# Optimization experiments

Measured on AMD Instinct MI355X. Metric: run time of the kernel, lower is better.

The kernel has to match this reference:

```python
import jax, jax.numpy as jnp
import numpy as np

L, B, S, D, H, FF, V, P = 6, 8, 1024, 768, 12, 3072, 50257, 1024
DH = D // H
EPS = 1e-5


def setup_inputs() -> dict:
    key = jax.random.key(0)
    ks = jax.random.split(key, 12)
    std = 0.02
    return {
        "x_ids": jax.random.randint(ks[0], (B, S), 0, V),
        "calibrated_mask": jax.random.normal(ks[1], (B, S, S), jnp.float32),
        "wte": jax.random.normal(ks[2], (V, D), jnp.float32) * std,
        "wpe": jax.random.normal(ks[3], (P, D), jnp.float32) * std,
        "ln1_g": jnp.ones((L, D), jnp.float32),
        "ln1_b": jnp.zeros((L, D), jnp.float32),
        "qkv_w": jax.random.normal(ks[4], (L, D, 3 * D), jnp.float32) * std,
        "qkv_b": jnp.zeros((L, 3 * D), jnp.float32),
        "ao_w": jax.random.normal(ks[5], (L, D, D), jnp.float32) * std,
        "ao_b": jnp.zeros((L, D), jnp.float32),
        "ln2_g": jnp.ones((L, D), jnp.float32),
        "ln2_b": jnp.zeros((L, D), jnp.float32),
        "fc_w": jax.random.normal(ks[6], (L, D, FF), jnp.float32) * std,
        "fc_b": jnp.zeros((L, FF), jnp.float32),
        "op_w": jax.random.normal(ks[7], (L, FF, D), jnp.float32) * std,
        "op_b": jnp.zeros((L, D), jnp.float32),
        "lnf_g": jnp.ones((D,), jnp.float32),
        "lnf_b": jnp.zeros((D,), jnp.float32),
    }


def _ln(x, g, b):
    m = jnp.mean(x, axis=-1, keepdims=True)
    v = jnp.var(x, axis=-1, keepdims=True)
    return (x - m) * jax.lax.rsqrt(v + EPS) * g + b


def _gelu_new(x):
    c = np.sqrt(2.0 / np.pi).astype(np.float32)
    return 0.5 * x * (1.0 + jnp.tanh(c * (x + 0.044715 * x * x * x)))


def _gpt2_forward(x_ids, calibrated_mask, wte, wpe, ln1_g, ln1_b, qkv_w, qkv_b,
                  ao_w, ao_b, ln2_g, ln2_b, fc_w, fc_b, op_w, op_b, lnf_g, lnf_b):
    s = x_ids.shape[1]
    h = wte[x_ids] + wpe[:s][None, :, :]  # [B,S,D]
    causal = jnp.tril(jnp.ones((s, s), bool))
    neg = jnp.finfo(h.dtype).min
    # additive mask, broadcast over heads (unsqueeze(1).repeat over n_head)
    add_mask = calibrated_mask[:, None, :, :]  # [B,1,S,S]

    def block(hid, p):
        l1g, l1b, qw, qb, aw, ab, l2g, l2b, fw, fb, ow, ob = p
        x = _ln(hid, l1g, l1b)
        qkv = x @ qw + qb  # [B,S,3D]
        q, k, v = jnp.split(qkv, 3, axis=-1)
        q = q.reshape(q.shape[0], s, H, DH).transpose(0, 2, 1, 3)
        k = k.reshape(k.shape[0], s, H, DH).transpose(0, 2, 1, 3)
        v = v.reshape(v.shape[0], s, H, DH).transpose(0, 2, 1, 3)
        scores = jnp.einsum('bhqd,bhkd->bhqk', q, k) / jnp.sqrt(jnp.asarray(DH, q.dtype))
        scores = jnp.where(causal[None, None], scores, neg)
        scores = scores + add_mask
        w = jax.nn.softmax(scores, axis=-1)
        a = jnp.einsum('bhqk,bhkd->bhqd', w, v)
        a = a.transpose(0, 2, 1, 3).reshape(a.shape[0], s, D)
        hid = hid + a @ aw + ab
        x2 = _ln(hid, l2g, l2b)
        hid = hid + _gelu_new(x2 @ fw + fb) @ ow + ob
        return hid, None

    params = (ln1_g, ln1_b, qkv_w, qkv_b, ao_w, ao_b, ln2_g, ln2_b, fc_w, fc_b, op_w, op_b)
    h, _ = jax.lax.scan(block, h, params)
    return _ln(h, lnf_g, lnf_b)


def reference(x_ids, calibrated_mask, wte, wpe, ln1_g, ln1_b, qkv_w, qkv_b,
              ao_w, ao_b, ln2_g, ln2_b, fc_w, fc_b, op_w, op_b, lnf_g, lnf_b):
    return _gpt2_forward(x_ids, calibrated_mask, wte, wpe, ln1_g, ln1_b, qkv_w, qkv_b,
                         ao_w, ao_b, ln2_g, ln2_b, fc_w, fc_b, op_w, op_b, lnf_g, lnf_b)
```

## Files before the change

### kernel.cpp

```cpp
#include <hip/hip_runtime.h>
#include <hip/hip_bf16.h>

typedef __bf16 bf16_t;
typedef __bf16 bf16x8 __attribute__((ext_vector_type(8)));
typedef float  f32x4  __attribute__((ext_vector_type(4)));

#define DEV __device__ __forceinline__

DEV void gload_lds16(const void* g, void* l) {
  __builtin_amdgcn_global_load_lds(
      (__attribute__((address_space(1))) void*)(void*)g,
      (__attribute__((address_space(3))) void*)l, 16, 0, 0);
}

__global__ __launch_bounds__(256)
void transpose_cast(const float* __restrict__ in, bf16_t* __restrict__ out,
                    int K, int N) {
  __shared__ float tile[32][33];
  const int k0 = blockIdx.x * 32;
  const int n0 = blockIdx.y * 32;
  const int tx = threadIdx.x;
  const int ty = threadIdx.y;
#pragma unroll
  for (int i = 0; i < 32; i += 8)
    tile[ty + i][tx] = in[(long)(k0 + ty + i) * N + n0 + tx];
  __syncthreads();
#pragma unroll
  for (int i = 0; i < 32; i += 8)
    out[(long)(n0 + ty + i) * K + k0 + tx] = (bf16_t)tile[tx][ty + i];
}

__global__ __launch_bounds__(256)
void embed_kernel(const int* __restrict__ ids, const float* __restrict__ wte,
                  const float* __restrict__ wpe, float* __restrict__ h) {
  const int idx = blockIdx.x * 256 + threadIdx.x;
  const int col = idx % 768;
  const int row = idx / 768;
  const int s   = row & 1023;
  h[idx] = wte[(long)ids[row] * 768 + col] + wpe[s * 768 + col];
}

template <bool BF16OUT>
__global__ __launch_bounds__(256)
void ln_kernel(const float* __restrict__ x, const float* __restrict__ g,
               const float* __restrict__ b, bf16_t* __restrict__ ob,
               float* __restrict__ of) {
  const long row = blockIdx.x;
  const float* xr = x + row * 768;
  const int t = threadIdx.x;
  float v0 = xr[t], v1 = xr[t + 256], v2 = xr[t + 512];
  float s  = v0 + v1 + v2;
  float sq = v0 * v0 + v1 * v1 + v2 * v2;
#pragma unroll
  for (int o = 32; o; o >>= 1) { s += __shfl_down(s, o); sq += __shfl_down(sq, o); }
  __shared__ float red[8];
  const int w = t >> 6;
  if ((t & 63) == 0) { red[w] = s; red[4 + w] = sq; }
  __syncthreads();
  s  = red[0] + red[1] + red[2] + red[3];
  sq = red[4] + red[5] + red[6] + red[7];
  const float mean = s * (1.f / 768.f);
  const float rs = rsqrtf(sq * (1.f / 768.f) - mean * mean + 1e-5f);
  float vv[3] = {v0, v1, v2};
#pragma unroll
  for (int i = 0; i < 3; ++i) {
    const int col = t + i * 256;
    const float o2 = (vv[i] - mean) * rs * g[col] + b[col];
    if (BF16OUT) ob[row * 768 + col] = (bf16_t)o2;
    else         of[row * 768 + col] = o2;
  }
}

template <int EPI, int BN>
__global__ __launch_bounds__(256, 4)
void gemm_bt(const bf16_t* __restrict__ A, const bf16_t* __restrict__ Bt,
             const float* __restrict__ bias, float* __restrict__ Cf,
             bf16_t* __restrict__ Cb, int M, int N, int K) {
  constexpr int NI = BN / 32;
  __shared__ bf16_t As[128 * 64];
  __shared__ bf16_t Bs[BN * 64];
  const int tid  = threadIdx.x;
  const int lane = tid & 63, w = tid >> 6;
  const int col = lane & 15, s16 = lane >> 4;
  const int nbn = N / BN;
  const int cpx = gridDim.x >> 3;
  const int bid = (blockIdx.x & 7) * cpx + (blockIdx.x >> 3);
  const int bm = bid / nbn, bn = bid % nbn;
  const int wr = w >> 1, wc = w & 1;

  f32x4 acc[4][NI];
#pragma unroll
  for (int i = 0; i < 4; ++i)
#pragma unroll
    for (int j = 0; j < NI; ++j) acc[i][j] = f32x4{0.f, 0.f, 0.f, 0.f};

  const long arow0 = (long)bm * 128;
  const long brow0 = (long)bn * BN;

  const int nt = K >> 6;
  for (int t = 0; t < nt; ++t) {
    const int k0 = t << 6;
#pragma unroll
    for (int i = 0; i < 4; ++i) {
      const int c = i * 256 + tid;
      const int row = c >> 3, slot = c & 7;
      gload_lds16(A + (arow0 + row) * (long)K + k0 + ((slot ^ (row & 7)) << 3),
                  (char*)As + c * 16);
    }
#pragma unroll
    for (int i = 0; i < BN / 32; ++i) {
      const int c = i * 256 + tid;
      const int row = c >> 3, slot = c & 7;
      gload_lds16(Bt + (brow0 + row) * (long)K + k0 + ((slot ^ (row & 7)) << 3),
                  (char*)Bs + c * 16);
    }
    __syncthreads();

    bf16x8 af[2][4], bfr[2][NI];
#pragma unroll
    for (int mi = 0; mi < 4; ++mi) {
      const int row = wr * 64 + mi * 16 + col;
#pragma unroll
      for (int ks = 0; ks < 2; ++ks) {
        const int slot = ks * 4 + s16;
        af[ks][mi] = *(const bf16x8*)((char*)As + row * 128 +
                                      ((slot ^ (row & 7)) << 4));
      }
    }
#pragma unroll
    for (int ni = 0; ni < NI; ++ni) {
      const int row = wc * (BN / 2) + ni * 16 + col;
#pragma unroll
      for (int ks = 0; ks < 2; ++ks) {
        const int slot = ks * 4 + s16;
        bfr[ks][ni] = *(const bf16x8*)((char*)Bs + row * 128 +
                                       ((slot ^ (row & 7)) << 4));
      }
    }
#pragma unroll
    for (int ks = 0; ks < 2; ++ks)
#pragma unroll
      for (int mi = 0; mi < 4; ++mi)
#pragma unroll
        for (int ni = 0; ni < NI; ++ni)
          acc[mi][ni] = __builtin_amdgcn_mfma_f32_16x16x32_bf16(
              af[ks][mi], bfr[ks][ni], acc[mi][ni], 0, 0, 0);

    __syncthreads();
  }

  const int colb = bn * BN + wc * (BN / 2) + col;
  const int rowb = bm * 128 + wr * 64 + (s16 << 2);
#pragma unroll
  for (int ni = 0; ni < NI; ++ni) {
    const int ccol = colb + ni * 16;
    const float bv = bias[ccol];
#pragma unroll
    for (int mi = 0; mi < 4; ++mi) {
      const int row = rowb + mi * 16;
#pragma unroll
      for (int r = 0; r < 4; ++r) {
        const float v = acc[mi][ni][r] + bv;
        const long idx = (long)(row + r) * N + ccol;
        if (EPI == 0)      Cf[idx] = v;
        else if (EPI == 1) Cf[idx] += v;
        else if (EPI == 2) Cb[idx] = (bf16_t)v;
        else {
          const float z = 0.7978845608028654f * (v + 0.044715f * v * v * v);
          Cb[idx] = (bf16_t)(v / (1.f + __expf(-2.f * z)));
        }
      }
    }
  }
}

template <int EPI>
__global__ __launch_bounds__(512, 4)
void gemm_wide(const bf16_t* __restrict__ A, const bf16_t* __restrict__ Bt,
               const float* __restrict__ bias, float* __restrict__ Cf,
               bf16_t* __restrict__ Cb, int M, int N, int K) {
  __shared__ bf16_t As[128 * 64];
  __shared__ bf16_t Bs[256 * 64];
  const int tid = threadIdx.x;
  const int lane = tid & 63, w = tid >> 6;
  const int col = lane & 15, s16 = lane >> 4;
  const int wm = w >> 2, wn = w & 3;
  const int nbn = N >> 8;
  const int cpx = gridDim.x >> 3;
  const int bid = (blockIdx.x & 7) * cpx + (blockIdx.x >> 3);
  const int bm = bid / nbn, bn = bid % nbn;
  const long arow0 = (long)bm * 128, brow0 = (long)bn * 256;

  f32x4 acc[4][4];
#pragma unroll
  for (int i = 0; i < 4; ++i)
#pragma unroll
    for (int j = 0; j < 4; ++j) acc[i][j] = f32x4{0.f, 0.f, 0.f, 0.f};

  const int nt = K >> 6;
  for (int t = 0; t < nt; ++t) {
    const int k0 = t << 6;
#pragma unroll
    for (int i = 0; i < 2; ++i) {
      const int c = i * 512 + tid;
      const int row = c >> 3, slot = c & 7;
      gload_lds16(A + (arow0 + row) * (long)K + k0 + ((slot ^ (row & 7)) << 3),
                  (char*)As + c * 16);
    }
#pragma unroll
    for (int i = 0; i < 4; ++i) {
      const int c = i * 512 + tid;
      const int row = c >> 3, slot = c & 7;
      gload_lds16(Bt + (brow0 + row) * (long)K + k0 + ((slot ^ (row & 7)) << 3),
                  (char*)Bs + c * 16);
    }
    __syncthreads();

    bf16x8 af[2][4], bfr[2][4];
#pragma unroll
    for (int mi = 0; mi < 4; ++mi) {
      const int row = wm * 64 + mi * 16 + col;
#pragma unroll
      for (int ks = 0; ks < 2; ++ks) {
        const int slot = ks * 4 + s16;
        af[ks][mi] = *(const bf16x8*)((char*)As + row * 128 +
                                      ((slot ^ (row & 7)) << 4));
      }
    }
#pragma unroll
    for (int ni = 0; ni < 4; ++ni) {
      const int row = wn * 64 + ni * 16 + col;
#pragma unroll
      for (int ks = 0; ks < 2; ++ks) {
        const int slot = ks * 4 + s16;
        bfr[ks][ni] = *(const bf16x8*)((char*)Bs + row * 128 +
                                       ((slot ^ (row & 7)) << 4));
      }
    }
#pragma unroll
    for (int ks = 0; ks < 2; ++ks)
#pragma unroll
      for (int mi = 0; mi < 4; ++mi)
#pragma unroll
        for (int ni = 0; ni < 4; ++ni)
          acc[mi][ni] = __builtin_amdgcn_mfma_f32_16x16x32_bf16(
              af[ks][mi], bfr[ks][ni], acc[mi][ni], 0, 0, 0);

    __syncthreads();
  }

  const int rowb = bm * 128 + wm * 64 + (s16 << 2);
  const int colb = bn * 256 + wn * 64 + col;
#pragma unroll
  for (int ni = 0; ni < 4; ++ni) {
    const int ccol = colb + ni * 16;
    const float bv = bias[ccol];
#pragma unroll
    for (int mi = 0; mi < 4; ++mi) {
      const int row = rowb + mi * 16;
#pragma unroll
      for (int r = 0; r < 4; ++r) {
        const float v = acc[mi][ni][r] + bv;
        const long idx = (long)(row + r) * N + ccol;
        if (EPI == 2) Cb[idx] = (bf16_t)v;
        else {
          const float z = 0.7978845608028654f * (v + 0.044715f * v * v * v);
          Cb[idx] = (bf16_t)(v / (1.f + __expf(-2.f * z)));
        }
      }
    }
  }
}

__global__ __launch_bounds__(256, 3)
void attn_kernel(const bf16_t* __restrict__ qkv, const float* __restrict__ mask,
                 bf16_t* __restrict__ out) {
  __shared__ bf16_t Kl[2][64 * 64];
  __shared__ bf16_t Vt[2][64 * 64];
  __shared__ bf16_t Pl[4][16 * 64];
  const int tid = threadIdx.x, lane = tid & 63, w = tid >> 6;
  const int col = lane & 15, s16 = lane >> 4, l7 = lane & 7;
  const int qp = blockIdx.x & 7;
  const int bh = blockIdx.x >> 3;
  const int b = bh / 12, h = bh % 12;
  const int sw0 = (s16 ^ l7) << 4;
  const int sw1 = ((s16 + 4) ^ l7) << 4;
  char* const plw = (char*)&Pl[w][0];
  const long qkvb = (long)b * 1024 * 2304;

  auto stageK = [&](int buf, int k0) {
#pragma unroll
    for (int i = 0; i < 2; ++i) {
      const int c = i * 256 + tid;
      const int krow = c >> 3, slot = c & 7;
      gload_lds16(qkv + qkvb + (long)(k0 + krow) * 2304 + 768 + h * 64 +
                      ((slot ^ (krow & 7)) << 3),
                  (char*)&Kl[buf][0] + i * 4096 + w * 1024);
    }
  };
  auto loadV = [&](int k0, bf16x8& t0, bf16x8& t1) {
    const bf16_t* vbase = qkv + qkvb + 1536 + h * 64;
#pragma unroll
    for (int i = 0; i < 2; ++i) {
      const int c = i * 256 + tid;
      const int d = c & 63, koct = c >> 6;
      const bf16_t* vsrc = vbase + (long)(k0 + koct * 8) * 2304 + d;
      bf16x8 tv;
#pragma unroll
      for (int j = 0; j < 8; ++j) tv[j] = vsrc[(long)j * 2304];
      if (i == 0) t0 = tv; else t1 = tv;
    }
  };
  auto storeV = [&](int buf, const bf16x8& t0, const bf16x8& t1) {
#pragma unroll
    for (int i = 0; i < 2; ++i) {
      const int c = i * 256 + tid;
      const int d = c & 63, koct = c >> 6;
      *(bf16x8*)((char*)&Vt[buf][0] + d * 128 + ((koct ^ (d & 7)) << 4)) =
          (i == 0) ? t0 : t1;
    }
  };

#pragma unroll 1
  for (int pass = 0; pass < 2; ++pass) {
    const int qt = pass ? (15 - qp) : qp;
    const int qrow0 = qt * 64 + w * 16;
    const long rowQ = (long)(b * 1024 + qrow0 + col) * 2304 + h * 64;
    const bf16x8 aq0 = *(const bf16x8*)&qkv[rowQ + s16 * 8];
    const bf16x8 aq1 = *(const bf16x8*)&qkv[rowQ + 32 + s16 * 8];
    const int qb = qrow0 + s16 * 4;
    const float* mrow = mask + ((long)b * 1024 + qb) * 1024;

    auto loadM = [&](int k0, float (&m)[4][4]) {
#pragma unroll
      for (int g = 0; g < 4; ++g)
#pragma unroll
        for (int r = 0; r < 4; ++r)
          m[g][r] = mrow[(long)r * 1024 + k0 + g * 16 + col];
    };

    float m_run[4], l_run[4];
    f32x4 o_acc[4];
#pragma unroll
    for (int r = 0; r < 4; ++r) { m_run[r] = -INFINITY; l_run[r] = 0.f; }
#pragma unroll
    for (int go = 0; go < 4; ++go) o_acc[go] = f32x4{0.f, 0.f, 0.f, 0.f};

    bf16x8 tv0, tv1;
    stageK(0, 0);
    loadV(0, tv0, tv1);
    storeV(0, tv0, tv1);
    float msk[4][4];
    loadM(0, msk);
    __syncthreads();

#pragma unroll 1
    for (int kt = 0; kt <= qt; ++kt) {
      const int cur = kt & 1;
      const bool more = kt < qt;
      const int k0 = kt * 64;
      float mnx[4][4];
      if (more) {
        stageK(cur ^ 1, k0 + 64);
        loadV(k0 + 64, tv0, tv1);
        loadM(k0 + 64, mnx);
      }

      f32x4 sf[4];
      __builtin_amdgcn_s_setprio(1);
#pragma unroll
      for (int g = 0; g < 4; ++g) {
        const int rbyte = (g * 16 + col) * 128;
        bf16x8 bk0 = *(const bf16x8*)((char*)&Kl[cur][0] + rbyte + sw0);
        bf16x8 bk1 = *(const bf16x8*)((char*)&Kl[cur][0] + rbyte + sw1);
        f32x4 z = f32x4{0.f, 0.f, 0.f, 0.f};
        z = __builtin_amdgcn_mfma_f32_16x16x32_bf16(aq0, bk0, z, 0, 0, 0);
        z = __builtin_amdgcn_mfma_f32_16x16x32_bf16(aq1, bk1, z, 0, 0, 0);
        sf[g] = z;
      }
      __builtin_amdgcn_s_setprio(0);

      const bool diag = (kt == qt);
      float sv[4][4];
#pragma unroll
      for (int g = 0; g < 4; ++g)
#pragma unroll
        for (int r = 0; r < 4; ++r) {
          float s = sf[g][r] * 0.125f + msk[g][r];
          if (diag && (k0 + g * 16 + col) > (qb + r)) s = -INFINITY;
          sv[g][r] = s;
        }
#pragma unroll
      for (int r = 0; r < 4; ++r) {
        float mx = fmaxf(fmaxf(sv[0][r], sv[1][r]), fmaxf(sv[2][r], sv[3][r]));
#pragma unroll
        for (int o = 8; o; o >>= 1) mx = fmaxf(mx, __shfl_xor(mx, o));
        const float m_new = fmaxf(m_run[r], mx);
        const float f = __expf(m_run[r] - m_new);
        m_run[r] = m_new;
        float sum = 0.f;
#pragma unroll
        for (int g = 0; g < 4; ++g) {
          const float p = __expf(sv[g][r] - m_new);
          sv[g][r] = p;
          sum += p;
        }
#pragma unroll
        for (int o = 8; o; o >>= 1) sum += __shfl_xor(sum, o);
        l_run[r] = l_run[r] * f + sum;
#pragma unroll
        for (int go = 0; go < 4; ++go) o_acc[go][r] *= f;
      }

#pragma unroll
      for (int g = 0; g < 4; ++g) {
        const int ks = 2 * g + (col >> 3);
#pragma unroll
        for (int r = 0; r < 4; ++r) {
          const int qr = s16 * 4 + r;
          *(bf16_t*)(plw + qr * 128 + ((ks ^ (qr & 7)) << 4) + l7 * 2) = (bf16_t)sv[g][r];
        }
      }
      const bf16x8 pa0 = *(const bf16x8*)(plw + col * 128 + sw0);
      const bf16x8 pa1 = *(const bf16x8*)(plw + col * 128 + sw1);
      __builtin_amdgcn_s_setprio(1);
#pragma unroll
      for (int go = 0; go < 4; ++go) {
        const int dbyte = (go * 16 + col) * 128;
        bf16x8 bv0 = *(const bf16x8*)((char*)&Vt[cur][0] + dbyte + sw0);
        bf16x8 bv1 = *(const bf16x8*)((char*)&Vt[cur][0] + dbyte + sw1);
        o_acc[go] = __builtin_amdgcn_mfma_f32_16x16x32_bf16(pa0, bv0, o_acc[go], 0, 0, 0);
        o_acc[go] = __builtin_amdgcn_mfma_f32_16x16x32_bf16(pa1, bv1, o_acc[go], 0, 0, 0);
      }
      __builtin_amdgcn_s_setprio(0);

      if (more) {
        storeV(cur ^ 1, tv0, tv1);
#pragma unroll
        for (int g = 0; g < 4; ++g)
#pragma unroll
          for (int r = 0; r < 4; ++r) msk[g][r] = mnx[g][r];
      }
      __syncthreads();
    }

    float inv[4];
#pragma unroll
    for (int r = 0; r < 4; ++r) inv[r] = 1.f / l_run[r];
#pragma unroll
    for (int go = 0; go < 4; ++go)
#pragma unroll
      for (int r = 0; r < 4; ++r)
        out[(long)(b * 1024 + qb + r) * 768 + h * 64 + go * 16 + col] =
            (bf16_t)(o_acc[go][r] * inv[r]);
  }
}

extern "C" void kernel_launch(void* const* d_in, const int* in_sizes, int n_in,
                              void* d_out, int out_size, void* d_ws, size_t ws_size,
                              hipStream_t stream) {
  const int*   x_ids = (const int*)d_in[0];
  const float* mask  = (const float*)d_in[1];
  const float* wte   = (const float*)d_in[2];
  const float* wpe   = (const float*)d_in[3];
  const float* ln1_g = (const float*)d_in[4];
  const float* ln1_b = (const float*)d_in[5];
  const float* qkv_w = (const float*)d_in[6];
  const float* qkv_b = (const float*)d_in[7];
  const float* ao_w  = (const float*)d_in[8];
  const float* ao_b  = (const float*)d_in[9];
  const float* ln2_g = (const float*)d_in[10];
  const float* ln2_b = (const float*)d_in[11];
  const float* fc_w  = (const float*)d_in[12];
  const float* fc_b  = (const float*)d_in[13];
  const float* op_w  = (const float*)d_in[14];
  const float* op_b  = (const float*)d_in[15];
  const float* lnf_g = (const float*)d_in[16];
  const float* lnf_b = (const float*)d_in[17];

  char* ws = (char*)d_ws;
  size_t off = 0;
  auto alloc = [&](size_t bytes) {
    char* p = ws + off;
    off += (bytes + 255) & ~(size_t)255;
    return p;
  };
  bf16_t* wqT = (bf16_t*)alloc(6ull * 2304 * 768 * 2);
  bf16_t* waT = (bf16_t*)alloc(6ull * 768 * 768 * 2);
  bf16_t* wfT = (bf16_t*)alloc(6ull * 3072 * 768 * 2);
  bf16_t* woT = (bf16_t*)alloc(6ull * 768 * 3072 * 2);
  float*  h   = (float*) alloc(8192ull * 768 * 4);
  bf16_t* xb  = (bf16_t*)alloc(8192ull * 768 * 2);
  bf16_t* qkv = (bf16_t*)alloc(8192ull * 2304 * 2);
  bf16_t* abf = (bf16_t*)alloc(8192ull * 768 * 2);
  bf16_t* fb  = (bf16_t*)alloc(8192ull * 3072 * 2);
  if (off > ws_size) return;

  const dim3 tb(32, 8);
  for (int l = 0; l < 6; ++l) {
    transpose_cast<<<dim3(768 / 32, 2304 / 32), tb, 0, stream>>>(
        qkv_w + (long)l * 768 * 2304, wqT + (long)l * 2304 * 768, 768, 2304);
    transpose_cast<<<dim3(768 / 32, 768 / 32), tb, 0, stream>>>(
        ao_w + (long)l * 768 * 768, waT + (long)l * 768 * 768, 768, 768);
    transpose_cast<<<dim3(768 / 32, 3072 / 32), tb, 0, stream>>>(
        fc_w + (long)l * 768 * 3072, wfT + (long)l * 3072 * 768, 768, 3072);
    transpose_cast<<<dim3(3072 / 32, 768 / 32), tb, 0, stream>>>(
        op_w + (long)l * 3072 * 768, woT + (long)l * 768 * 3072, 3072, 768);
  }

  embed_kernel<<<24576, 256, 0, stream>>>(x_ids, wte, wpe, h);

  for (int l = 0; l < 6; ++l) {
    ln_kernel<true><<<8192, 256, 0, stream>>>(h, ln1_g + l * 768, ln1_b + l * 768, xb, nullptr);
    gemm_wide<2><<<576, 512, 0, stream>>>(xb, wqT + (long)l * 2304 * 768,
                                          qkv_b + l * 2304, nullptr, qkv, 8192, 2304, 768);
    attn_kernel<<<768, 256, 0, stream>>>(qkv, mask, abf);
    gemm_bt<1, 64><<<768, 256, 0, stream>>>(abf, waT + (long)l * 768 * 768,
                                            ao_b + l * 768, h, nullptr, 8192, 768, 768);
    ln_kernel<true><<<8192, 256, 0, stream>>>(h, ln2_g + l * 768, ln2_b + l * 768, xb, nullptr);
    gemm_wide<3><<<768, 512, 0, stream>>>(xb, wfT + (long)l * 3072 * 768,
                                          fc_b + l * 3072, nullptr, fb, 8192, 3072, 768);
    gemm_bt<1, 64><<<768, 256, 0, stream>>>(fb, woT + (long)l * 768 * 3072,
                                            op_b + l * 768, h, nullptr, 8192, 768, 3072);
  }

  ln_kernel<false><<<8192, 256, 0, stream>>>(h, lnf_g, lnf_b, nullptr, (float*)d_out);
}
```

Before: 1.738 ms.

## Replace wide GEMM with double-buffered 256x192 tile kernel for QKV and FC

Replaces the 128x256-tile, 512-thread GEMM used for the QKV and FC projections with a 256x192-tile, 384-thread (6-wave) kernel. Each wave now computes a 128x64 output block, and LDS is double-buffered so the next K-slice is staged while MFMAs run on the current one. This aims to raise operand reuse per LDS load and overlap global loads with compute. The cost is more accumulator registers (32 f32x4) and about 112KB of LDS per block, which lowers occupancy. The grid shrinks to 384 and 512 blocks, which may underfill the 256 CUs in the tail.

```diff
diff --git a/kernel.cpp b/kernel.cpp
--- a/kernel.cpp
+++ b/kernel.cpp
@@ -175,97 +175,105 @@
 }
 
 template <int EPI>
-__global__ __launch_bounds__(512, 4)
-void gemm_wide(const bf16_t* __restrict__ A, const bf16_t* __restrict__ Bt,
-               const float* __restrict__ bias, float* __restrict__ Cf,
-               bf16_t* __restrict__ Cb, int M, int N, int K) {
-  __shared__ bf16_t As[128 * 64];
-  __shared__ bf16_t Bs[256 * 64];
+__global__ __launch_bounds__(384)
+void gemm192(const bf16_t* __restrict__ A, const bf16_t* __restrict__ Bt,
+             const float* __restrict__ bias, bf16_t* __restrict__ Cb,
+             int M, int N, int K) {
+  __shared__ bf16_t As[2][256 * 64];
+  __shared__ bf16_t Bs[2][192 * 64];
   const int tid = threadIdx.x;
   const int lane = tid & 63, w = tid >> 6;
   const int col = lane & 15, s16 = lane >> 4;
-  const int wm = w >> 2, wn = w & 3;
-  const int nbn = N >> 8;
+  const int wm = w / 3, wn = w % 3;
+  const int nbn = N / 192;
   const int cpx = gridDim.x >> 3;
   const int bid = (blockIdx.x & 7) * cpx + (blockIdx.x >> 3);
   const int bm = bid / nbn, bn = bid % nbn;
-  const long arow0 = (long)bm * 128, brow0 = (long)bn * 256;
-
-  f32x4 acc[4][4];
-#pragma unroll
-  for (int i = 0; i < 4; ++i)
+  const long arow0 = (long)bm * 256, brow0 = (long)bn * 192;
+
+  f32x4 acc[8][4];
+#pragma unroll
+  for (int i = 0; i < 8; ++i)
 #pragma unroll
     for (int j = 0; j < 4; ++j) acc[i][j] = f32x4{0.f, 0.f, 0.f, 0.f};
 
-  const int nt = K >> 6;
-  for (int t = 0; t < nt; ++t) {
-    const int k0 = t << 6;
-#pragma unroll
-    for (int i = 0; i < 2; ++i) {
-      const int c = i * 512 + tid;
-      const int row = c >> 3, slot = c & 7;
-      gload_lds16(A + (arow0 + row) * (long)K + k0 + ((slot ^ (row & 7)) << 3),
-                  (char*)As + c * 16);
+  auto stage = [&](int buf, int k0) {
+#pragma unroll
+    for (int i = 0; i < 6; ++i) {
+      const int c = i * 384 + tid;
+      if (c < 2048) {
+        const int row = c >> 3, slot = c & 7;
+        gload_lds16(A + (arow0 + row) * (long)K + k0 + ((slot ^ (row & 7)) << 3),
+                    (char*)&As[buf][0] + c * 16);
+      }
     }
 #pragma unroll
     for (int i = 0; i < 4; ++i) {
-      const int c = i * 512 + tid;
+      const int c = i * 384 + tid;
       const int row = c >> 3, slot = c & 7;
       gload_lds16(Bt + (brow0 + row) * (long)K + k0 + ((slot ^ (row & 7)) << 3),
-                  (char*)Bs + c * 16);
-    }
-    __syncthreads();
-
-    bf16x8 af[2][4], bfr[2][4];
-#pragma unroll
-    for (int mi = 0; mi < 4; ++mi) {
-      const int row = wm * 64 + mi * 16 + col;
-#pragma unroll
-      for (int ks = 0; ks < 2; ++ks) {
-        const int slot = ks * 4 + s16;
-        af[ks][mi] = *(const bf16x8*)((char*)As + row * 128 +
-                                      ((slot ^ (row & 7)) << 4));
-      }
-    }
+                  (char*)&Bs[buf][0] + c * 16);
+    }
+  };
+
+  const int nt = K >> 6;
+  stage(0, 0);
+  __syncthreads();
+  int cur = 0;
+
+  for (int t = 0; t < nt; ++t) {
+    if (t + 1 < nt) stage(cur ^ 1, (t + 1) << 6);
+
+    bf16x8 bfr[2][4];
 #pragma unroll
     for (int ni = 0; ni < 4; ++ni) {
       const int row = wn * 64 + ni * 16 + col;
 #pragma unroll
-      for (int ks = 0; ks < 2; ++ks) {
-        const int slot = ks * 4 + s16;
-        bfr[ks][ni] = *(const bf16x8*)((char*)Bs + row * 128 +
-                                       ((slot ^ (row & 7)) << 4));
-      }
-    }
-#pragma unroll
-    for (int ks = 0; ks < 2; ++ks)
-#pragma unroll
-      for (int mi = 0; mi < 4; ++mi)
-#pragma unroll
-        for (int ni = 0; ni < 4; ++ni)
-          acc[mi][ni] = __builtin_amdgcn_mfma_f32_16x16x32_bf16(
-              af[ks][mi], bfr[ks][ni], acc[mi][ni], 0, 0, 0);
+      for (int ks = 0; ks < 2; ++ks)
+        bfr[ks][ni] = *(const bf16x8*)((char*)&Bs[cur][0] + row * 128 +
+                                       (((ks * 4 + s16) ^ (row & 7)) << 4));
+    }
+#pragma unroll
+    for (int mh = 0; mh < 2; ++mh) {
+      bf16x8 af[2][4];
+#pragma unroll
+      for (int mi = 0; mi < 4; ++mi) {
+        const int row = wm * 128 + mh * 64 + mi * 16 + col;
+#pragma unroll
+        for (int ks = 0; ks < 2; ++ks)
+          af[ks][mi] = *(const bf16x8*)((char*)&As[cur][0] + row * 128 +
+                                        (((ks * 4 + s16) ^ (row & 7)) << 4));
+      }
+#pragma unroll
+      for (int ks = 0; ks < 2; ++ks)
+#pragma unroll
+        for (int mi = 0; mi < 4; ++mi)
+#pragma unroll
+          for (int ni = 0; ni < 4; ++ni)
+            acc[mh * 4 + mi][ni] = __builtin_amdgcn_mfma_f32_16x16x32_bf16(
+                af[ks][mi], bfr[ks][ni], acc[mh * 4 + mi][ni], 0, 0, 0);
+    }
 
     __syncthreads();
-  }
-
-  const int rowb = bm * 128 + wm * 64 + (s16 << 2);
-  const int colb = bn * 256 + wn * 64 + col;
+    cur ^= 1;
+  }
+
+  const int rowb = bm * 256 + wm * 128 + (s16 << 2);
+  const int colb = bn * 192 + wn * 64 + col;
 #pragma unroll
   for (int ni = 0; ni < 4; ++ni) {
     const int ccol = colb + ni * 16;
     const float bv = bias[ccol];
 #pragma unroll
-    for (int mi = 0; mi < 4; ++mi) {
-      const int row = rowb + mi * 16;
+    for (int m = 0; m < 8; ++m) {
+      const int row = rowb + m * 16;
 #pragma unroll
       for (int r = 0; r < 4; ++r) {
-        const float v = acc[mi][ni][r] + bv;
-        const long idx = (long)(row + r) * N + ccol;
-        if (EPI == 2) Cb[idx] = (bf16_t)v;
+        const float v = acc[m][ni][r] + bv;
+        if (EPI == 2) Cb[(long)(row + r) * N + ccol] = (bf16_t)v;
         else {
           const float z = 0.7978845608028654f * (v + 0.044715f * v * v * v);
-          Cb[idx] = (bf16_t)(v / (1.f + __expf(-2.f * z)));
+          Cb[(long)(row + r) * N + ccol] = (bf16_t)(v / (1.f + __expf(-2.f * z)));
         }
       }
     }
@@ -512,14 +520,14 @@
 
   for (int l = 0; l < 6; ++l) {
     ln_kernel<true><<<8192, 256, 0, stream>>>(h, ln1_g + l * 768, ln1_b + l * 768, xb, nullptr);
-    gemm_wide<2><<<576, 512, 0, stream>>>(xb, wqT + (long)l * 2304 * 768,
-                                          qkv_b + l * 2304, nullptr, qkv, 8192, 2304, 768);
+    gemm192<2><<<384, 384, 0, stream>>>(xb, wqT + (long)l * 2304 * 768,
+                                        qkv_b + l * 2304, qkv, 8192, 2304, 768);
     attn_kernel<<<768, 256, 0, stream>>>(qkv, mask, abf);
     gemm_bt<1, 64><<<768, 256, 0, stream>>>(abf, waT + (long)l * 768 * 768,
                                             ao_b + l * 768, h, nullptr, 8192, 768, 768);
     ln_kernel<true><<<8192, 256, 0, stream>>>(h, ln2_g + l * 768, ln2_b + l * 768, xb, nullptr);
-    gemm_wide<3><<<768, 512, 0, stream>>>(xb, wfT + (long)l * 3072 * 768,
-                                          fc_b + l * 3072, nullptr, fb, 8192, 3072, 768);
+    gemm192<3><<<512, 384, 0, stream>>>(xb, wfT + (long)l * 3072 * 768,
+                                        fc_b + l * 3072, fb, 8192, 3072, 768);
     gemm_bt<1, 64><<<768, 256, 0, stream>>>(fb, woT + (long)l * 768 * 3072,
                                             op_b + l * 768, h, nullptr, 8192, 768, 3072);
   }
```

After: 1.920 ms. 1.1x slower.

## Store residual stream in bf16 and move FC GEMM to gemm_bt tile

Applied to the files above, without the earlier changes.

The residual hidden state buffer changes from fp32 to bf16, so embed, layernorm reads and the residual-add epilogues all work on half the bytes. The FC1+GELU GEMM moves from the 512-thread wide kernel to gemm_bt with a 128-wide N tile and 1536 blocks, and gemm_wide keeps only the plain bias epilogue. Accumulating the residual in bf16 across 12 additions lowers accuracy and risks exceeding tolerance.

```diff
diff --git a/kernel.cpp b/kernel.cpp
--- a/kernel.cpp
+++ b/kernel.cpp
@@ -32,23 +32,23 @@
 
 __global__ __launch_bounds__(256)
 void embed_kernel(const int* __restrict__ ids, const float* __restrict__ wte,
-                  const float* __restrict__ wpe, float* __restrict__ h) {
+                  const float* __restrict__ wpe, bf16_t* __restrict__ h) {
   const int idx = blockIdx.x * 256 + threadIdx.x;
   const int col = idx % 768;
   const int row = idx / 768;
   const int s   = row & 1023;
-  h[idx] = wte[(long)ids[row] * 768 + col] + wpe[s * 768 + col];
+  h[idx] = (bf16_t)(wte[(long)ids[row] * 768 + col] + wpe[s * 768 + col]);
 }
 
 template <bool BF16OUT>
 __global__ __launch_bounds__(256)
-void ln_kernel(const float* __restrict__ x, const float* __restrict__ g,
+void ln_kernel(const bf16_t* __restrict__ x, const float* __restrict__ g,
                const float* __restrict__ b, bf16_t* __restrict__ ob,
                float* __restrict__ of) {
   const long row = blockIdx.x;
-  const float* xr = x + row * 768;
+  const bf16_t* xr = x + row * 768;
   const int t = threadIdx.x;
-  float v0 = xr[t], v1 = xr[t + 256], v2 = xr[t + 512];
+  float v0 = (float)xr[t], v1 = (float)xr[t + 256], v2 = (float)xr[t + 512];
   float s  = v0 + v1 + v2;
   float sq = v0 * v0 + v1 * v1 + v2 * v2;
 #pragma unroll
@@ -74,8 +74,8 @@
 template <int EPI, int BN>
 __global__ __launch_bounds__(256, 4)
 void gemm_bt(const bf16_t* __restrict__ A, const bf16_t* __restrict__ Bt,
-             const float* __restrict__ bias, float* __restrict__ Cf,
-             bf16_t* __restrict__ Cb, int M, int N, int K) {
+             const float* __restrict__ bias, bf16_t* __restrict__ Cb,
+             int M, int N, int K) {
   constexpr int NI = BN / 32;
   __shared__ bf16_t As[128 * 64];
   __shared__ bf16_t Bs[BN * 64];
@@ -162,10 +162,11 @@
       for (int r = 0; r < 4; ++r) {
         const float v = acc[mi][ni][r] + bv;
         const long idx = (long)(row + r) * N + ccol;
-        if (EPI == 0)      Cf[idx] = v;
-        else if (EPI == 1) Cf[idx] += v;
-        else if (EPI == 2) Cb[idx] = (bf16_t)v;
-        else {
+        if (EPI == 1) {
+          Cb[idx] = (bf16_t)((float)Cb[idx] + v);
+        } else if (EPI == 2) {
+          Cb[idx] = (bf16_t)v;
+        } else {
           const float z = 0.7978845608028654f * (v + 0.044715f * v * v * v);
           Cb[idx] = (bf16_t)(v / (1.f + __expf(-2.f * z)));
         }
@@ -174,11 +175,10 @@
   }
 }
 
-template <int EPI>
 __global__ __launch_bounds__(512, 4)
 void gemm_wide(const bf16_t* __restrict__ A, const bf16_t* __restrict__ Bt,
-               const float* __restrict__ bias, float* __restrict__ Cf,
-               bf16_t* __restrict__ Cb, int M, int N, int K) {
+               const float* __restrict__ bias, bf16_t* __restrict__ Cb,
+               int M, int N, int K) {
   __shared__ bf16_t As[128 * 64];
   __shared__ bf16_t Bs[256 * 64];
   const int tid = threadIdx.x;
@@ -259,15 +259,8 @@
     for (int mi = 0; mi < 4; ++mi) {
       const int row = rowb + mi * 16;
 #pragma unroll
-      for (int r = 0; r < 4; ++r) {
-        const float v = acc[mi][ni][r] + bv;
-        const long idx = (long)(row + r) * N + ccol;
-        if (EPI == 2) Cb[idx] = (bf16_t)v;
-        else {
-          const float z = 0.7978845608028654f * (v + 0.044715f * v * v * v);
-          Cb[idx] = (bf16_t)(v / (1.f + __expf(-2.f * z)));
-        }
-      }
+      for (int r = 0; r < 4; ++r)
+        Cb[(long)(row + r) * N + ccol] = (bf16_t)(acc[mi][ni][r] + bv);
     }
   }
 }
@@ -489,7 +482,7 @@
   bf16_t* waT = (bf16_t*)alloc(6ull * 768 * 768 * 2);
   bf16_t* wfT = (bf16_t*)alloc(6ull * 3072 * 768 * 2);
   bf16_t* woT = (bf16_t*)alloc(6ull * 768 * 3072 * 2);
-  float*  h   = (float*) alloc(8192ull * 768 * 4);
+  bf16_t* h   = (bf16_t*)alloc(8192ull * 768 * 2);
   bf16_t* xb  = (bf16_t*)alloc(8192ull * 768 * 2);
   bf16_t* qkv = (bf16_t*)alloc(8192ull * 2304 * 2);
   bf16_t* abf = (bf16_t*)alloc(8192ull * 768 * 2);
@@ -512,16 +505,16 @@
 
   for (int l = 0; l < 6; ++l) {
     ln_kernel<true><<<8192, 256, 0, stream>>>(h, ln1_g + l * 768, ln1_b + l * 768, xb, nullptr);
-    gemm_wide<2><<<576, 512, 0, stream>>>(xb, wqT + (long)l * 2304 * 768,
-                                          qkv_b + l * 2304, nullptr, qkv, 8192, 2304, 768);
+    gemm_wide<<<576, 512, 0, stream>>>(xb, wqT + (long)l * 2304 * 768,
+                                       qkv_b + l * 2304, qkv, 8192, 2304, 768);
     attn_kernel<<<768, 256, 0, stream>>>(qkv, mask, abf);
     gemm_bt<1, 64><<<768, 256, 0, stream>>>(abf, waT + (long)l * 768 * 768,
-                                            ao_b + l * 768, h, nullptr, 8192, 768, 768);
+                                            ao_b + l * 768, h, 8192, 768, 768);
     ln_kernel<true><<<8192, 256, 0, stream>>>(h, ln2_g + l * 768, ln2_b + l * 768, xb, nullptr);
-    gemm_wide<3><<<768, 512, 0, stream>>>(xb, wfT + (long)l * 3072 * 768,
-                                          fc_b + l * 3072, nullptr, fb, 8192, 3072, 768);
+    gemm_bt<3, 128><<<1536, 256, 0, stream>>>(xb, wfT + (long)l * 3072 * 768,
+                                              fc_b + l * 3072, fb, 8192, 3072, 768);
     gemm_bt<1, 64><<<768, 256, 0, stream>>>(fb, woT + (long)l * 768 * 3072,
-                                            op_b + l * 768, h, nullptr, 8192, 768, 3072);
+                                            op_b + l * 768, h, 8192, 768, 3072);
   }
 
   ln_kernel<false><<<8192, 256, 0, stream>>>(h, lnf_g, lnf_b, nullptr, (float*)d_out);
```

Result: faster. 1.652 ms (-4.9%).
